# Performance work log

Measured on AMD Instinct MI355X. Metric: run time of the kernel, lower is better.

## Reference

```python
import jax, jax.numpy as jnp
import numpy as np

N, D, E, TOPK = 16384, 4096, 64, 8
NOISE_EPS = 0.01


def setup_inputs() -> dict:
    key = jax.random.key(0)
    kx, kw, kn = jax.random.split(key, 3)
    x = jax.random.normal(kx, (N, D), dtype=jnp.float32)
    W = jax.random.normal(kw, (D, E), dtype=jnp.float32) * 0.02  # gate weight (Linear, no bias)
    noise = jax.random.normal(kn, (N, E), dtype=jnp.float32) * NOISE_EPS  # training-mode gate noise
    return {"x": x, "W": W, "noise": noise, "top_k": TOPK}


def reference(x, W, noise, top_k):
    # logits -> noisy logits -> softmax gates
    gates = jax.nn.softmax(x @ W + noise, axis=-1)          # [N, E]
    top_k_gates, top_k_indices = jax.lax.top_k(gates, top_k)  # [N, k] each
    top_k_gates = top_k_gates / jnp.sum(top_k_gates, axis=-1, keepdims=True)
    # load-balancing aux loss (training path), vectorized over experts
    num_experts = W.shape[1]
    importance = jnp.mean(gates, axis=0)                     # [E]
    load = jnp.zeros((num_experts,), gates.dtype).at[top_k_indices.reshape(-1)].add(1.0)
    load = load / top_k_indices.size                         # mean of (indices == i) over N*k
    load_balancing_loss = jnp.sum(importance * load) * num_experts
    return top_k_gates, top_k_indices, load_balancing_loss
```

## Files before the change

kernel.cpp:

```cpp
#include <hip/hip_runtime.h>

#define NROWS 16384
#define DDIM  4096
#define NEXP  64
#define TAU   1e-3f
#define KSP   4
#define CB    2048
#define RB    2048
#define RBLK  64

typedef __attribute__((ext_vector_type(8))) short bf16x8;
typedef __attribute__((ext_vector_type(4))) float f32x4;

__device__ __forceinline__ ushort f2bf(float f) {
    uint u = __float_as_uint(f);
    u += 0x7FFFu + ((u >> 16) & 1u);
    return (ushort)(u >> 16);
}
__device__ __forceinline__ float bf2f(ushort h) {
    return __uint_as_float(((uint)h) << 16);
}
__device__ __forceinline__ void cvt8(const float4& a, const float4& b,
                                     bf16x8& H, bf16x8& L) {
    const float v[8] = {a.x, a.y, a.z, a.w, b.x, b.y, b.z, b.w};
    #pragma unroll
    for (int i = 0; i < 8; ++i) {
        const ushort h = f2bf(v[i]);
        H[i] = (short)h;
        L[i] = (short)f2bf(v[i] - bf2f(h));
    }
}

__global__ __launch_bounds__(256) void wprep(
    const float* __restrict__ Wg, ushort* __restrict__ wfrag)
{
    const int gid  = (int)blockIdx.x * 256 + threadIdx.x;
    const int lane = gid & 63, frag = gid >> 6;
    const int nt = frag & 3, ks = (frag >> 2) & 1, tg = frag >> 3;
    const int k0 = tg * 64 + ks * 32 + (lane >> 4) * 8;
    const int e  = nt * 16 + (lane & 15);
    bf16x8 H, L;
    #pragma unroll
    for (int j = 0; j < 8; ++j) {
        const float v = Wg[(size_t)(k0 + j) * NEXP + e];
        const ushort h = f2bf(v);
        H[j] = (short)h;
        L[j] = (short)f2bf(v - bf2f(h));
    }
    *(bf16x8*)&wfrag[((size_t)frag * 2 + 0) * 512 + lane * 8] = H;
    *(bf16x8*)&wfrag[((size_t)frag * 2 + 1) * 512 + lane * 8] = L;
}

__global__ __launch_bounds__(256, 4) void gemm_mfma(
    const float* __restrict__ x, const ushort* __restrict__ wfrag,
    float* __restrict__ partials, int* __restrict__ counter)
{
    if (blockIdx.x == 0 && threadIdx.x == 0) *counter = 0;

    __shared__ ushort wbuf[2][8192];

    const int tid  = threadIdx.x;
    const int lane = tid & 63;
    const int w    = tid >> 6;
    const int rb   = (int)blockIdx.x >> 2;
    const int kq   = (int)blockIdx.x & 3;
    const int fr   = lane & 15;
    const int q    = lane >> 4;

    const float*  xp   = x + (size_t)(rb * 64 + w * 16 + fr) * DDIM
                           + kq * 1024 + q * 8;
    const ushort* wsrc = wfrag + (size_t)(kq * 16) * 8192 + tid * 8;

    f32x4 acc[4];
    #pragma unroll
    for (int nt = 0; nt < 4; ++nt) acc[nt] = (f32x4){0.f, 0.f, 0.f, 0.f};

    uint4 wst[4];
    #pragma unroll
    for (int c = 0; c < 4; ++c)
        wst[c] = *(const uint4*)(wsrc + c * 2048);
    #pragma unroll
    for (int c = 0; c < 4; ++c)
        *(uint4*)&wbuf[0][c * 2048 + tid * 8] = wst[c];
    float4 c0a = *(const float4*)(xp);
    float4 c0b = *(const float4*)(xp + 4);
    float4 c1a = *(const float4*)(xp + 32);
    float4 c1b = *(const float4*)(xp + 36);
    __syncthreads();

    int cur = 0;
    for (int t = 0; t < 16; ++t) {
        float4 n0a, n0b, n1a, n1b;
        if (t + 1 < 16) {
            #pragma unroll
            for (int c = 0; c < 4; ++c)
                wst[c] = *(const uint4*)(wsrc + (size_t)(t + 1) * 8192 + c * 2048);
            const float* xn = xp + (t + 1) * 64;
            n0a = *(const float4*)(xn);
            n0b = *(const float4*)(xn + 4);
            n1a = *(const float4*)(xn + 32);
            n1b = *(const float4*)(xn + 36);
        }

        bf16x8 ah0, al0, ah1, al1;
        cvt8(c0a, c0b, ah0, al0);
        cvt8(c1a, c1b, ah1, al1);

        const ushort* wt = &wbuf[cur][0];
        #pragma unroll
        for (int ks = 0; ks < 2; ++ks) {
            const bf16x8 a_h = ks ? ah1 : ah0;
            const bf16x8 a_l = ks ? al1 : al0;
            #pragma unroll
            for (int nt = 0; nt < 4; ++nt) {
                const bf16x8 w_h =
                    *(const bf16x8*)&wt[((ks * 4 + nt) * 2 + 0) * 512 + lane * 8];
                const bf16x8 w_l =
                    *(const bf16x8*)&wt[((ks * 4 + nt) * 2 + 1) * 512 + lane * 8];
                acc[nt] = __builtin_amdgcn_mfma_f32_16x16x32_bf16(a_h, w_h, acc[nt], 0, 0, 0);
                acc[nt] = __builtin_amdgcn_mfma_f32_16x16x32_bf16(a_h, w_l, acc[nt], 0, 0, 0);
                acc[nt] = __builtin_amdgcn_mfma_f32_16x16x32_bf16(a_l, w_h, acc[nt], 0, 0, 0);
            }
        }

        if (t + 1 < 16) {
            #pragma unroll
            for (int c = 0; c < 4; ++c)
                *(uint4*)&wbuf[cur ^ 1][c * 2048 + tid * 8] = wst[c];
            c0a = n0a; c0b = n0b; c1a = n1a; c1b = n1b;
        }
        __syncthreads();
        cur ^= 1;
    }

    float* po = partials + ((size_t)kq * NROWS + rb * 64 + w * 16) * 64;
    #pragma unroll
    for (int nt = 0; nt < 4; ++nt)
        #pragma unroll
        for (int r = 0; r < 4; ++r)
            po[(q * 4 + r) * 64 + nt * 16 + fr] = acc[nt][r];
}

__global__ __launch_bounds__(256) void combine_epilogue(
    const float* __restrict__ partials, const float* __restrict__ noise,
    float* __restrict__ out_gates, float* __restrict__ out_idx,
    float* __restrict__ ws_imp, float* __restrict__ ws_load,
    int* __restrict__ worklist, int* __restrict__ counter)
{
    __shared__ float red[4][NEXP];
    const int tid = threadIdx.x, lane = tid & 63, w = tid >> 6;

    float impacc = 0.f, loadacc = 0.f;
    #pragma unroll
    for (int rr = 0; rr < 2; ++rr) {
        const int grow = (int)blockIdx.x * 8 + w * 2 + rr;
        float v = noise[(size_t)grow * NEXP + lane];
        #pragma unroll
        for (int qq = 0; qq < KSP; ++qq)
            v += partials[(size_t)qq * NROWS * 64 + (size_t)grow * 64 + lane];

        float m = v;
        #pragma unroll
        for (int off = 32; off; off >>= 1) m = fmaxf(m, __shfl_xor(m, off));
        const float ex = __expf(v - m);
        float s = ex;
        #pragma unroll
        for (int off = 32; off; off >>= 1) s += __shfl_xor(s, off);
        const float g = ex * (1.0f / s);
        impacc += g;

        float work = v, vprev = 0.f;
        float myv = 0.f, sumtop = 0.f;
        int myi = 0, mine = 0, flg = 0;
        #pragma unroll
        for (int j = 0; j < 9; ++j) {
            float bv = work, bg = g; int bi = lane;
            #pragma unroll
            for (int off = 32; off; off >>= 1) {
                const float ov = __shfl_xor(bv, off);
                const int   oi = __shfl_xor(bi, off);
                const float og = __shfl_xor(bg, off);
                if (ov > bv || (ov == bv && oi < bi)) { bv = ov; bi = oi; bg = og; }
            }
            if (j > 0) flg |= (vprev - bv < TAU) ? 1 : 0;
            vprev = bv;
            if (j < 8) {
                sumtop += bg;
                if (lane == j)  { myv = bg; myi = bi; }
                if (lane == bi) { work = -3e38f; mine = 1; }
            }
        }
        loadacc += (float)mine;

        if (lane < 8) {
            out_gates[(size_t)grow * 8 + lane] = myv / sumtop;
            out_idx  [(size_t)grow * 8 + lane] = (float)myi;
        }
        if (lane == 0 && flg) {
            const int pos = atomicAdd(counter, 1);
            worklist[pos] = grow;
        }
    }

    red[w][lane] = impacc;
    __syncthreads();
    if (w == 0)
        ws_imp[(size_t)blockIdx.x * NEXP + lane] =
            red[0][lane] + red[1][lane] + red[2][lane] + red[3][lane];
    __syncthreads();
    red[w][lane] = loadacc;
    __syncthreads();
    if (w == 0)
        ws_load[(size_t)blockIdx.x * NEXP + lane] =
            red[0][lane] + red[1][lane] + red[2][lane] + red[3][lane];
}

__global__ __launch_bounds__(256) void reduce_stage(
    const float* __restrict__ ws_imp, const float* __restrict__ ws_load,
    float* __restrict__ st_imp, float* __restrict__ st_load)
{
    __shared__ float si[4][NEXP], sl[4][NEXP];
    const int tid = threadIdx.x, e = tid & 63, sub = tid >> 6;
    float a = 0.f, b = 0.f;
    #pragma unroll
    for (int i = 0; i < 8; ++i) {
        const int blk = (int)blockIdx.x * 32 + sub * 8 + i;
        a += ws_imp[(size_t)blk * NEXP + e];
        b += ws_load[(size_t)blk * NEXP + e];
    }
    si[sub][e] = a; sl[sub][e] = b;
    __syncthreads();
    if (sub == 0) {
        st_imp [(size_t)blockIdx.x * NEXP + e] = si[0][e] + si[1][e] + si[2][e] + si[3][e];
        st_load[(size_t)blockIdx.x * NEXP + e] = sl[0][e] + sl[1][e] + sl[2][e] + sl[3][e];
    }
}

__global__ __launch_bounds__(256) void repair_finalize(
    const float* __restrict__ x, const float* __restrict__ Wg,
    const float* __restrict__ noise, const int* __restrict__ worklist,
    const int* __restrict__ counter, const float* __restrict__ st_imp,
    const float* __restrict__ st_load, float* __restrict__ out_gates,
    float* __restrict__ out_idx, float* __restrict__ loss_out)
{
    const int tid = threadIdx.x, lane = tid & 63, w = tid >> 6;

    if (blockIdx.x == RB) {
        __shared__ float si[4][NEXP], sl[4][NEXP];
        float a = 0.f, b = 0.f;
        #pragma unroll
        for (int j = 0; j < RBLK / 4; ++j) {
            const int blk = w * (RBLK / 4) + j;
            a += st_imp[(size_t)blk * NEXP + lane];
            b += st_load[(size_t)blk * NEXP + lane];
        }
        si[w][lane] = a; sl[w][lane] = b;
        __syncthreads();
        if (w == 0) {
            const float imp = (si[0][lane] + si[1][lane] + si[2][lane] + si[3][lane])
                              / (float)NROWS;
            const float ld  = (sl[0][lane] + sl[1][lane] + sl[2][lane] + sl[3][lane])
                              / (float)(NROWS * 8);
            float term = imp * ld;
            #pragma unroll
            for (int off = 32; off; off >>= 1) term += __shfl_xor(term, off);
            if (lane == 0) *loss_out = term * (float)NEXP;
        }
        return;
    }

    __shared__ float xr[DDIM];
    __shared__ double red64[4][NEXP];
    const int count = *counter;

    for (int i = (int)blockIdx.x; i < count; i += RB) {
        const int grow = worklist[i];
        __syncthreads();
        #pragma unroll
        for (int qq = 0; qq < 4; ++qq)
            ((float4*)xr)[tid + 256 * qq] =
                ((const float4*)(x + (size_t)grow * DDIM))[tid + 256 * qq];
        __syncthreads();

        double ch[8];
        #pragma unroll
        for (int c = 0; c < 8; ++c) ch[c] = 0.0;
        const float* wp = Wg + (size_t)(w * 1024) * NEXP + lane;
        const float* xq = xr + w * 1024;
        #pragma unroll 4
        for (int k = 0; k < 1024; k += 8) {
            #pragma unroll
            for (int c = 0; c < 8; ++c)
                ch[c] = fma((double)xq[k + c],
                            (double)wp[(size_t)(k + c) * NEXP], ch[c]);
        }
        red64[w][lane] = (((ch[0] + ch[1]) + (ch[2] + ch[3]))
                        + ((ch[4] + ch[5]) + (ch[6] + ch[7])));
        __syncthreads();

        if (w == 0) {
            const double v64 = (((red64[0][lane] + red64[1][lane]) + red64[2][lane])
                                + red64[3][lane]) + (double)noise[(size_t)grow * NEXP + lane];
            double m = v64;
            #pragma unroll
            for (int off = 32; off; off >>= 1) m = fmax(m, __shfl_xor(m, off));
            const float ex = __expf((float)(v64 - m));
            float s = ex;
            #pragma unroll
            for (int off = 32; off; off >>= 1) s += __shfl_xor(s, off);
            const float g = ex * (1.0f / s);

            double work = v64;
            float myv = 0.f, sumtop = 0.f, bg;
            int myi = 0;
            #pragma unroll
            for (int j = 0; j < 8; ++j) {
                double bv = work; int bi = lane; bg = g;
                #pragma unroll
                for (int off = 32; off; off >>= 1) {
                    const double ov = __shfl_xor(bv, off);
                    const int    oi = __shfl_xor(bi, off);
                    const float  og = __shfl_xor(bg, off);
                    if (ov > bv || (ov == bv && oi < bi)) { bv = ov; bi = oi; bg = og; }
                }
                sumtop += bg;
                if (lane == j)  { myv = bg; myi = bi; }
                if (lane == bi) work = -1e300;
            }
            if (lane < 8) {
                out_gates[(size_t)grow * 8 + lane] = myv / sumtop;
                out_idx  [(size_t)grow * 8 + lane] = (float)myi;
            }
        }
    }
}

extern "C" void kernel_launch(void* const* d_in, const int* in_sizes, int n_in,
                              void* d_out, int out_size, void* d_ws, size_t ws_size,
                              hipStream_t stream) {
    const float* x     = (const float*)d_in[0];
    const float* Wg    = (const float*)d_in[1];
    const float* noise = (const float*)d_in[2];
    float* out       = (float*)d_out;
    float* out_gates = out;
    float* out_idx   = out + (size_t)NROWS * 8;
    float* loss_out  = out + (size_t)2 * NROWS * 8;

    ushort* wfrag   = (ushort*)d_ws;
    float* partials = (float*)(wfrag + (size_t)1048576);
    float* ws_imp   = partials + (size_t)KSP * NROWS * 64;
    float* ws_load  = ws_imp + (size_t)CB * NEXP;
    float* st_imp   = ws_load + (size_t)CB * NEXP;
    float* st_load  = st_imp + (size_t)RBLK * NEXP;
    int*   worklist = (int*)(st_load + (size_t)RBLK * NEXP);
    int*   counter  = worklist + NROWS;

    wprep          <<<128,       256, 0, stream>>>(Wg, wfrag);
    gemm_mfma      <<<256 * KSP, 256, 0, stream>>>(x, wfrag, partials, counter);
    combine_epilogue<<<CB,       256, 0, stream>>>(partials, noise, out_gates, out_idx,
                                                   ws_imp, ws_load, worklist, counter);
    reduce_stage   <<<RBLK,      256, 0, stream>>>(ws_imp, ws_load, st_imp, st_load);
    repair_finalize<<<RB + 1,    256, 0, stream>>>(x, Wg, noise, worklist, counter,
                                                   st_imp, st_load, out_gates, out_idx,
                                                   loss_out);
}
```

Before: 149.2 us.

## Halve GEMM split-K factor and process two K-chunks per pipeline step

Reduces the split-K factor from 4 to 2, so each GEMM block covers 2048 of K and each loop iteration handles two 64-wide K chunks with a doubled shared-memory weight buffer. This halves the partial-sum traffic written to and re-read from global memory, and gives deeper per-iteration prefetch. In exchange there are only 512 blocks, occupancy is lower, and each block uses more registers and LDS. The counter reset moves into the wprep kernel.

```diff
diff --git a/kernel.cpp b/kernel.cpp
--- a/kernel.cpp
+++ b/kernel.cpp
@@ -4,7 +4,7 @@
 #define DDIM  4096
 #define NEXP  64
 #define TAU   1e-3f
-#define KSP   4
+#define KSP   2
 #define CB    2048
 #define RB    2048
 #define RBLK  64
@@ -32,8 +32,10 @@
 }
 
 __global__ __launch_bounds__(256) void wprep(
-    const float* __restrict__ Wg, ushort* __restrict__ wfrag)
-{
+    const float* __restrict__ Wg, ushort* __restrict__ wfrag,
+    int* __restrict__ counter)
+{
+    if (blockIdx.x == 0 && threadIdx.x == 0) *counter = 0;
     const int gid  = (int)blockIdx.x * 256 + threadIdx.x;
     const int lane = gid & 63, frag = gid >> 6;
     const int nt = frag & 3, ks = (frag >> 2) & 1, tg = frag >> 3;
@@ -51,83 +53,95 @@
     *(bf16x8*)&wfrag[((size_t)frag * 2 + 1) * 512 + lane * 8] = L;
 }
 
-__global__ __launch_bounds__(256, 4) void gemm_mfma(
+__global__ __launch_bounds__(256, 2) void gemm_mfma(
     const float* __restrict__ x, const ushort* __restrict__ wfrag,
-    float* __restrict__ partials, int* __restrict__ counter)
-{
-    if (blockIdx.x == 0 && threadIdx.x == 0) *counter = 0;
-
-    __shared__ ushort wbuf[2][8192];
+    float* __restrict__ partials)
+{
+    __shared__ ushort wbuf[2][16384];
 
     const int tid  = threadIdx.x;
     const int lane = tid & 63;
     const int w    = tid >> 6;
-    const int rb   = (int)blockIdx.x >> 2;
-    const int kq   = (int)blockIdx.x & 3;
+    const int rb   = (int)blockIdx.x >> 1;
+    const int kq   = (int)blockIdx.x & 1;
     const int fr   = lane & 15;
     const int q    = lane >> 4;
 
     const float*  xp   = x + (size_t)(rb * 64 + w * 16 + fr) * DDIM
-                           + kq * 1024 + q * 8;
-    const ushort* wsrc = wfrag + (size_t)(kq * 16) * 8192 + tid * 8;
+                           + kq * 2048 + q * 8;
+    const ushort* wsrc = wfrag + (size_t)(kq * 32) * 8192 + tid * 8;
 
     f32x4 acc[4];
     #pragma unroll
     for (int nt = 0; nt < 4; ++nt) acc[nt] = (f32x4){0.f, 0.f, 0.f, 0.f};
 
-    uint4 wst[4];
-    #pragma unroll
-    for (int c = 0; c < 4; ++c)
+    uint4 wst[8];
+    #pragma unroll
+    for (int c = 0; c < 8; ++c)
         wst[c] = *(const uint4*)(wsrc + c * 2048);
     #pragma unroll
-    for (int c = 0; c < 4; ++c)
+    for (int c = 0; c < 8; ++c)
         *(uint4*)&wbuf[0][c * 2048 + tid * 8] = wst[c];
-    float4 c0a = *(const float4*)(xp);
-    float4 c0b = *(const float4*)(xp + 4);
-    float4 c1a = *(const float4*)(xp + 32);
-    float4 c1b = *(const float4*)(xp + 36);
+    float4 cx[8];
+    #pragma unroll
+    for (int s = 0; s < 2; ++s) {
+        cx[s * 4 + 0] = *(const float4*)(xp + s * 64);
+        cx[s * 4 + 1] = *(const float4*)(xp + s * 64 + 4);
+        cx[s * 4 + 2] = *(const float4*)(xp + s * 64 + 32);
+        cx[s * 4 + 3] = *(const float4*)(xp + s * 64 + 36);
+    }
     __syncthreads();
 
     int cur = 0;
     for (int t = 0; t < 16; ++t) {
-        float4 n0a, n0b, n1a, n1b;
+        float4 nx[8];
         if (t + 1 < 16) {
             #pragma unroll
-            for (int c = 0; c < 4; ++c)
-                wst[c] = *(const uint4*)(wsrc + (size_t)(t + 1) * 8192 + c * 2048);
-            const float* xn = xp + (t + 1) * 64;
-            n0a = *(const float4*)(xn);
-            n0b = *(const float4*)(xn + 4);
-            n1a = *(const float4*)(xn + 32);
-            n1b = *(const float4*)(xn + 36);
-        }
-
-        bf16x8 ah0, al0, ah1, al1;
-        cvt8(c0a, c0b, ah0, al0);
-        cvt8(c1a, c1b, ah1, al1);
-
-        const ushort* wt = &wbuf[cur][0];
-        #pragma unroll
-        for (int ks = 0; ks < 2; ++ks) {
-            const bf16x8 a_h = ks ? ah1 : ah0;
-            const bf16x8 a_l = ks ? al1 : al0;
-            #pragma unroll
-            for (int nt = 0; nt < 4; ++nt) {
-                const bf16x8 w_h =
-                    *(const bf16x8*)&wt[((ks * 4 + nt) * 2 + 0) * 512 + lane * 8];
-                const bf16x8 w_l =
-                    *(const bf16x8*)&wt[((ks * 4 + nt) * 2 + 1) * 512 + lane * 8];
-                acc[nt] = __builtin_amdgcn_mfma_f32_16x16x32_bf16(a_h, w_h, acc[nt], 0, 0, 0);
-                acc[nt] = __builtin_amdgcn_mfma_f32_16x16x32_bf16(a_h, w_l, acc[nt], 0, 0, 0);
-                acc[nt] = __builtin_amdgcn_mfma_f32_16x16x32_bf16(a_l, w_h, acc[nt], 0, 0, 0);
+            for (int c = 0; c < 8; ++c)
+                wst[c] = *(const uint4*)(wsrc + (size_t)(t + 1) * 16384 + c * 2048);
+            const float* xn = xp + (t + 1) * 128;
+            #pragma unroll
+            for (int s = 0; s < 2; ++s) {
+                nx[s * 4 + 0] = *(const float4*)(xn + s * 64);
+                nx[s * 4 + 1] = *(const float4*)(xn + s * 64 + 4);
+                nx[s * 4 + 2] = *(const float4*)(xn + s * 64 + 32);
+                nx[s * 4 + 3] = *(const float4*)(xn + s * 64 + 36);
+            }
+        }
+
+        bf16x8 ah[4], al[4];
+        #pragma unroll
+        for (int s = 0; s < 2; ++s) {
+            cvt8(cx[s * 4 + 0], cx[s * 4 + 1], ah[s * 2 + 0], al[s * 2 + 0]);
+            cvt8(cx[s * 4 + 2], cx[s * 4 + 3], ah[s * 2 + 1], al[s * 2 + 1]);
+        }
+
+        #pragma unroll
+        for (int s = 0; s < 2; ++s) {
+            const ushort* wt = &wbuf[cur][s * 8192];
+            #pragma unroll
+            for (int ks = 0; ks < 2; ++ks) {
+                const bf16x8 a_h = ah[s * 2 + ks];
+                const bf16x8 a_l = al[s * 2 + ks];
+                #pragma unroll
+                for (int nt = 0; nt < 4; ++nt) {
+                    const bf16x8 w_h =
+                        *(const bf16x8*)&wt[((ks * 4 + nt) * 2 + 0) * 512 + lane * 8];
+                    const bf16x8 w_l =
+                        *(const bf16x8*)&wt[((ks * 4 + nt) * 2 + 1) * 512 + lane * 8];
+                    acc[nt] = __builtin_amdgcn_mfma_f32_16x16x32_bf16(a_h, w_h, acc[nt], 0, 0, 0);
+                    acc[nt] = __builtin_amdgcn_mfma_f32_16x16x32_bf16(a_h, w_l, acc[nt], 0, 0, 0);
+                    acc[nt] = __builtin_amdgcn_mfma_f32_16x16x32_bf16(a_l, w_h, acc[nt], 0, 0, 0);
+                }
             }
         }
 
         if (t + 1 < 16) {
             #pragma unroll
-            for (int c = 0; c < 4; ++c)
+            for (int c = 0; c < 8; ++c)
                 *(uint4*)&wbuf[cur ^ 1][c * 2048 + tid * 8] = wst[c];
-            c0a = n0a; c0b = n0b; c1a = n1a; c1b = n1b;
+            #pragma unroll
+            for (int c = 0; c < 8; ++c) cx[c] = nx[c];
         }
         __syncthreads();
         cur ^= 1;
@@ -355,8 +369,8 @@
     int*   worklist = (int*)(st_load + (size_t)RBLK * NEXP);
     int*   counter  = worklist + NROWS;
 
-    wprep          <<<128,       256, 0, stream>>>(Wg, wfrag);
-    gemm_mfma      <<<256 * KSP, 256, 0, stream>>>(x, wfrag, partials, counter);
+    wprep          <<<128,       256, 0, stream>>>(Wg, wfrag, counter);
+    gemm_mfma      <<<256 * KSP, 256, 0, stream>>>(x, wfrag, partials);
     combine_epilogue<<<CB,       256, 0, stream>>>(partials, noise, out_gates, out_idx,
                                                    ws_imp, ws_load, worklist, counter);
     reduce_stage   <<<RBLK,      256, 0, stream>>>(ws_imp, ws_load, st_imp, st_load);
```

Result: slower. 166.7 us (+11.7%).

## Process two 64-row subtiles per GEMM block to reuse W fragments

Applied to the files above, without the earlier changes.

Each GEMM block now handles 128 rows, with each wave computing two 16-row subtiles that share the W fragments loaded from LDS. The grid is halved and launch bounds lowered to allow more registers for the doubled accumulators and x prefetch. The counter reset moves into the weight-prep kernel. The aim is less LDS and global W traffic per row and more MFMA work per sync, at the cost of fewer resident waves to hide x-load latency.

```diff
diff --git a/kernel.cpp b/kernel.cpp
--- a/kernel.cpp
+++ b/kernel.cpp
@@ -32,8 +32,10 @@
 }
 
 __global__ __launch_bounds__(256) void wprep(
-    const float* __restrict__ Wg, ushort* __restrict__ wfrag)
-{
+    const float* __restrict__ Wg, ushort* __restrict__ wfrag,
+    int* __restrict__ counter)
+{
+    if (blockIdx.x == 0 && threadIdx.x == 0) *counter = 0;
     const int gid  = (int)blockIdx.x * 256 + threadIdx.x;
     const int lane = gid & 63, frag = gid >> 6;
     const int nt = frag & 3, ks = (frag >> 2) & 1, tg = frag >> 3;
@@ -51,12 +53,10 @@
     *(bf16x8*)&wfrag[((size_t)frag * 2 + 1) * 512 + lane * 8] = L;
 }
 
-__global__ __launch_bounds__(256, 4) void gemm_mfma(
+__global__ __launch_bounds__(256, 2) void gemm_mfma(
     const float* __restrict__ x, const ushort* __restrict__ wfrag,
-    float* __restrict__ partials, int* __restrict__ counter)
-{
-    if (blockIdx.x == 0 && threadIdx.x == 0) *counter = 0;
-
+    float* __restrict__ partials)
+{
     __shared__ ushort wbuf[2][8192];
 
     const int tid  = threadIdx.x;
@@ -67,13 +67,16 @@
     const int fr   = lane & 15;
     const int q    = lane >> 4;
 
-    const float*  xp   = x + (size_t)(rb * 64 + w * 16 + fr) * DDIM
-                           + kq * 1024 + q * 8;
+    const float* xp0 = x + (size_t)(rb * 128 + w * 16 + fr) * DDIM
+                         + kq * 1024 + q * 8;
+    const float* xp1 = xp0 + (size_t)64 * DDIM;
     const ushort* wsrc = wfrag + (size_t)(kq * 16) * 8192 + tid * 8;
 
-    f32x4 acc[4];
-    #pragma unroll
-    for (int nt = 0; nt < 4; ++nt) acc[nt] = (f32x4){0.f, 0.f, 0.f, 0.f};
+    f32x4 acc[2][4];
+    #pragma unroll
+    for (int st = 0; st < 2; ++st)
+        #pragma unroll
+        for (int nt = 0; nt < 4; ++nt) acc[st][nt] = (f32x4){0.f, 0.f, 0.f, 0.f};
 
     uint4 wst[4];
     #pragma unroll
@@ -82,44 +85,59 @@
     #pragma unroll
     for (int c = 0; c < 4; ++c)
         *(uint4*)&wbuf[0][c * 2048 + tid * 8] = wst[c];
-    float4 c0a = *(const float4*)(xp);
-    float4 c0b = *(const float4*)(xp + 4);
-    float4 c1a = *(const float4*)(xp + 32);
-    float4 c1b = *(const float4*)(xp + 36);
+    float4 cx[2][4];
+    #pragma unroll
+    for (int st = 0; st < 2; ++st) {
+        const float* xs = st ? xp1 : xp0;
+        cx[st][0] = *(const float4*)(xs);
+        cx[st][1] = *(const float4*)(xs + 4);
+        cx[st][2] = *(const float4*)(xs + 32);
+        cx[st][3] = *(const float4*)(xs + 36);
+    }
     __syncthreads();
 
     int cur = 0;
     for (int t = 0; t < 16; ++t) {
-        float4 n0a, n0b, n1a, n1b;
+        float4 nx[2][4];
         if (t + 1 < 16) {
             #pragma unroll
             for (int c = 0; c < 4; ++c)
                 wst[c] = *(const uint4*)(wsrc + (size_t)(t + 1) * 8192 + c * 2048);
-            const float* xn = xp + (t + 1) * 64;
-            n0a = *(const float4*)(xn);
-            n0b = *(const float4*)(xn + 4);
-            n1a = *(const float4*)(xn + 32);
-            n1b = *(const float4*)(xn + 36);
-        }
-
-        bf16x8 ah0, al0, ah1, al1;
-        cvt8(c0a, c0b, ah0, al0);
-        cvt8(c1a, c1b, ah1, al1);
+            #pragma unroll
+            for (int st = 0; st < 2; ++st) {
+                const float* xn = (st ? xp1 : xp0) + (t + 1) * 64;
+                nx[st][0] = *(const float4*)(xn);
+                nx[st][1] = *(const float4*)(xn + 4);
+                nx[st][2] = *(const float4*)(xn + 32);
+                nx[st][3] = *(const float4*)(xn + 36);
+            }
+        }
+
+        bf16x8 ah[2][2], al[2][2];
+        #pragma unroll
+        for (int st = 0; st < 2; ++st) {
+            cvt8(cx[st][0], cx[st][1], ah[st][0], al[st][0]);
+            cvt8(cx[st][2], cx[st][3], ah[st][1], al[st][1]);
+        }
 
         const ushort* wt = &wbuf[cur][0];
         #pragma unroll
         for (int ks = 0; ks < 2; ++ks) {
-            const bf16x8 a_h = ks ? ah1 : ah0;
-            const bf16x8 a_l = ks ? al1 : al0;
             #pragma unroll
             for (int nt = 0; nt < 4; ++nt) {
                 const bf16x8 w_h =
                     *(const bf16x8*)&wt[((ks * 4 + nt) * 2 + 0) * 512 + lane * 8];
                 const bf16x8 w_l =
                     *(const bf16x8*)&wt[((ks * 4 + nt) * 2 + 1) * 512 + lane * 8];
-                acc[nt] = __builtin_amdgcn_mfma_f32_16x16x32_bf16(a_h, w_h, acc[nt], 0, 0, 0);
-                acc[nt] = __builtin_amdgcn_mfma_f32_16x16x32_bf16(a_h, w_l, acc[nt], 0, 0, 0);
-                acc[nt] = __builtin_amdgcn_mfma_f32_16x16x32_bf16(a_l, w_h, acc[nt], 0, 0, 0);
+                #pragma unroll
+                for (int st = 0; st < 2; ++st) {
+                    acc[st][nt] = __builtin_amdgcn_mfma_f32_16x16x32_bf16(
+                        ah[st][ks], w_h, acc[st][nt], 0, 0, 0);
+                    acc[st][nt] = __builtin_amdgcn_mfma_f32_16x16x32_bf16(
+                        ah[st][ks], w_l, acc[st][nt], 0, 0, 0);
+                    acc[st][nt] = __builtin_amdgcn_mfma_f32_16x16x32_bf16(
+                        al[st][ks], w_h, acc[st][nt], 0, 0, 0);
+                }
             }
         }
 
@@ -127,18 +145,25 @@
             #pragma unroll
             for (int c = 0; c < 4; ++c)
                 *(uint4*)&wbuf[cur ^ 1][c * 2048 + tid * 8] = wst[c];
-            c0a = n0a; c0b = n0b; c1a = n1a; c1b = n1b;
+            #pragma unroll
+            for (int st = 0; st < 2; ++st)
+                #pragma unroll
+                for (int c = 0; c < 4; ++c) cx[st][c] = nx[st][c];
         }
         __syncthreads();
         cur ^= 1;
     }
 
-    float* po = partials + ((size_t)kq * NROWS + rb * 64 + w * 16) * 64;
-    #pragma unroll
-    for (int nt = 0; nt < 4; ++nt)
-        #pragma unroll
-        for (int r = 0; r < 4; ++r)
-            po[(q * 4 + r) * 64 + nt * 16 + fr] = acc[nt][r];
+    #pragma unroll
+    for (int st = 0; st < 2; ++st) {
+        float* po = partials
+                  + ((size_t)kq * NROWS + rb * 128 + st * 64 + w * 16) * 64;
+        #pragma unroll
+        for (int nt = 0; nt < 4; ++nt)
+            #pragma unroll
+            for (int r = 0; r < 4; ++r)
+                po[(q * 4 + r) * 64 + nt * 16 + fr] = acc[st][nt][r];
+    }
 }
 
 __global__ __launch_bounds__(256) void combine_epilogue(
@@ -355,12 +380,12 @@
     int*   worklist = (int*)(st_load + (size_t)RBLK * NEXP);
     int*   counter  = worklist + NROWS;
 
-    wprep          <<<128,       256, 0, stream>>>(Wg, wfrag);
-    gemm_mfma      <<<256 * KSP, 256, 0, stream>>>(x, wfrag, partials, counter);
-    combine_epilogue<<<CB,       256, 0, stream>>>(partials, noise, out_gates, out_idx,
-                                                   ws_imp, ws_load, worklist, counter);
-    reduce_stage   <<<RBLK,      256, 0, stream>>>(ws_imp, ws_load, st_imp, st_load);
-    repair_finalize<<<RB + 1,    256, 0, stream>>>(x, Wg, noise, worklist, counter,
-                                                   st_imp, st_load, out_gates, out_idx,
-                                                   loss_out);
-}
+    wprep          <<<128,    256, 0, stream>>>(Wg, wfrag, counter);
+    gemm_mfma      <<<512,    256, 0, stream>>>(x, wfrag, partials);
+    combine_epilogue<<<CB,    256, 0, stream>>>(partials, noise, out_gates, out_idx,
+                                                ws_imp, ws_load, worklist, counter);
+    reduce_stage   <<<RBLK,   256, 0, stream>>>(ws_imp, ws_load, st_imp, st_load);
+    repair_finalize<<<RB + 1, 256, 0, stream>>>(x, Wg, noise, worklist, counter,
+                                                st_imp, st_load, out_gates, out_idx,
+                                                loss_out);
+}
```

New measurement: 145.9 us. -2.2%, faster.
